# Kernel optimization log

Hardware: AMD Instinct MI355X
Metric: run time of the kernel (lower is better)

Reference implementation:

```python
import jax, jax.numpy as jnp
import numpy as np

K = 3  # hardcoded in TransitionUp.forward

def setup_inputs() -> dict:
    key = jax.random.key(0)
    ks = jax.random.split(key, 8)
    M, N = 32768, 8192
    UP_C, DOWN_C, OUT_C = 128, 256, 128
    return {
        "up_points": jax.random.normal(ks[0], (M, 3), dtype=jnp.float32),
        "up_features": jax.random.normal(ks[1], (M, UP_C), dtype=jnp.float32),
        "down_points": jax.random.normal(ks[2], (N, 3), dtype=jnp.float32),
        "down_features": jax.random.normal(ks[3], (N, DOWN_C), dtype=jnp.float32),
        # torch nn.Linear params: W [out,in], b [out]
        "W_up": jax.random.normal(ks[4], (OUT_C, UP_C), dtype=jnp.float32) / np.sqrt(UP_C),
        "b_up": jax.random.normal(ks[5], (OUT_C,), dtype=jnp.float32) * 0.01,
        "W_down": jax.random.normal(ks[6], (OUT_C, DOWN_C), dtype=jnp.float32) / np.sqrt(DOWN_C),
        "b_down": jax.random.normal(ks[7], (OUT_C,), dtype=jnp.float32) * 0.01,
    }

def interpolate_knn(query_points, dataset_points, dataset_features, k):
    # squared pairwise distances [M, N]
    delta = query_points[:, None, :] - dataset_points[None, :, :]
    dist = jnp.sum(delta * delta, axis=-1)
    neg_dist, knn_idx = jax.lax.top_k(-dist, k)  # smallest-k
    knn_dist = -neg_dist                           # [M, k]
    knn_feats = dataset_features[knn_idx]          # [M, k, C]
    recip = 1.0 / (knn_dist + 1e-8)
    weights = recip / jnp.sum(recip, axis=-1, keepdims=True)  # [M, k]
    return jnp.einsum('mk,mkc->mc', weights, knn_feats)

def reference(up_points, up_features, down_points, down_features, W_up, b_up, W_down, b_down):
    down_f = down_features @ W_down.T + b_down            # [N, OUT_C]
    interp_f = interpolate_knn(up_points, down_points, down_f, K)  # [M, OUT_C]
    return interp_f + (up_features @ W_up.T + b_up)
```

## Files before the change

### kernel.cpp

```cpp
#include <hip/hip_runtime.h>
#include <cfloat>

#define M_UP   32768
#define N_DOWN 8192
#define UPC    128
#define DOWNC  256
#define OUTC   128
#define NCHUNK 8
#define CHUNK  (N_DOWN / NCHUNK)
#define G      8
#define Q      2
#define PG     12

__device__ __forceinline__ void fma4(float4& acc, float s, const float4 w) {
    acc.x = fmaf(s, w.x, acc.x);
    acc.y = fmaf(s, w.y, acc.y);
    acc.z = fmaf(s, w.z, acc.z);
    acc.w = fmaf(s, w.w, acc.w);
}

__device__ __forceinline__ void top3_bl(float s, int idx,
                                        float& d0, float& d1, float& d2,
                                        int& i0, int& i1, int& i2) {
    bool c0 = s < d0, c1 = s < d1, c2 = s < d2;
    float n0 = fminf(d0, s);
    float n1 = __builtin_amdgcn_fmed3f(d0, d1, s);
    float n2 = __builtin_amdgcn_fmed3f(d1, d2, s);
    int m0 = c0 ? idx : i0;
    int m1 = c0 ? i0 : (c1 ? idx : i1);
    int m2 = c1 ? i1 : (c2 ? idx : i2);
    d0 = n0; d1 = n1; d2 = n2;
    i0 = m0; i1 = m1; i2 = m2;
}

__global__ __launch_bounds__(256) void transpose_w(
        const float* __restrict__ W_up, const float* __restrict__ W_down,
        float* __restrict__ wt_up, float* __restrict__ wt_down) {
    int e = blockIdx.x * 256 + threadIdx.x;
    if (e < DOWNC * OUTC) {
        int k = e >> 7, c = e & 127;
        wt_down[e] = W_down[c * DOWNC + k];
    } else {
        int e2 = e - DOWNC * OUTC;
        int k = e2 >> 7, c = e2 & 127;
        wt_up[e2] = W_up[c * UPC + k];
    }
}

__global__ __launch_bounds__(256) void down_proj(
        const float* __restrict__ A, const float* __restrict__ WT,
        const float* __restrict__ bias, float* __restrict__ down_f) {
    __shared__ __align__(16) float sA[16 * DOWNC];
    __shared__ __align__(16) float sW[64 * OUTC];
    {
        const float4* Ab4 = (const float4*)(A + blockIdx.x * 16 * DOWNC);
        float4* sA4 = (float4*)sA;
        #pragma unroll
        for (int i = 0; i < 4; ++i)
            sA4[threadIdx.x + i * 256] = Ab4[threadIdx.x + i * 256];
    }
    const int c4 = threadIdx.x & 31;
    const int rr = threadIdx.x >> 5;
    float4 acc0 = {0.f, 0.f, 0.f, 0.f};
    float4 acc1 = {0.f, 0.f, 0.f, 0.f};
    for (int kh = 0; kh < 4; ++kh) {
        if (kh) __syncthreads();
        {
            const float4* W4 = (const float4*)(WT + kh * 64 * OUTC);
            float4* sW4 = (float4*)sW;
            #pragma unroll
            for (int i = 0; i < 8; ++i)
                sW4[threadIdx.x + i * 256] = W4[threadIdx.x + i * 256];
        }
        __syncthreads();
        #pragma unroll 2
        for (int k2 = 0; k2 < 64; k2 += 4) {
            const int k = kh * 64 + k2;
            float4 a0 = *(const float4*)&sA[rr * DOWNC + k];
            float4 a1 = *(const float4*)&sA[(rr + 8) * DOWNC + k];
            const float4* wp = (const float4*)(sW + k2 * OUTC) + c4;
            float4 w0 = wp[0], w1 = wp[32], w2 = wp[64], w3 = wp[96];
            fma4(acc0, a0.x, w0); fma4(acc0, a0.y, w1);
            fma4(acc0, a0.z, w2); fma4(acc0, a0.w, w3);
            fma4(acc1, a1.x, w0); fma4(acc1, a1.y, w1);
            fma4(acc1, a1.z, w2); fma4(acc1, a1.w, w3);
        }
    }
    const int r0 = blockIdx.x * 16 + rr;
    const int r1 = r0 + 8;
    float4 b = ((const float4*)bias)[c4];
    acc0.x += b.x; acc0.y += b.y; acc0.z += b.z; acc0.w += b.w;
    acc1.x += b.x; acc1.y += b.y; acc1.z += b.z; acc1.w += b.w;
    ((float4*)down_f)[r0 * 32 + c4] = acc0;
    ((float4*)down_f)[r1 * 32 + c4] = acc1;
}

__global__ __launch_bounds__(256) void knn_partial(
        const float* __restrict__ up_points,
        const float* __restrict__ down_points,
        float2* __restrict__ part) {
    __shared__ __align__(16) float sx[PG * (CHUNK / G)];
    __shared__ __align__(16) float sy[PG * (CHUNK / G)];
    __shared__ __align__(16) float sz[PG * (CHUNK / G)];
    const int base = blockIdx.y * CHUNK;
    for (int t = threadIdx.x; t < CHUNK; t += 256) {
        int g = base + t;
        int gi = t >> 3, j = t & 7;
        sx[PG * gi + j] = down_points[3 * g];
        sy[PG * gi + j] = down_points[3 * g + 1];
        sz[PG * gi + j] = down_points[3 * g + 2];
    }
    __syncthreads();

    const int m0 = blockIdx.x * (256 * Q) + threadIdx.x;
    const int m1 = m0 + 256;
    const float q0x = up_points[3 * m0];
    const float q0y = up_points[3 * m0 + 1];
    const float q0z = up_points[3 * m0 + 2];
    const float q1x = up_points[3 * m1];
    const float q1y = up_points[3 * m1 + 1];
    const float q1z = up_points[3 * m1 + 2];

    float a_gd0 = FLT_MAX, a_gd1 = FLT_MAX, a_gd2 = FLT_MAX;
    int   a_gi0 = 0, a_gi1 = 0, a_gi2 = 0;
    float b_gd0 = FLT_MAX, b_gd1 = FLT_MAX, b_gd2 = FLT_MAX;
    int   b_gi0 = 0, b_gi1 = 0, b_gi2 = 0;

    for (int gi = 0; gi < CHUNK / G; ++gi) {
        float4 x0 = *(const float4*)&sx[PG * gi], x1 = *(const float4*)&sx[PG * gi + 4];
        float4 y0 = *(const float4*)&sy[PG * gi], y1 = *(const float4*)&sy[PG * gi + 4];
        float4 z0 = *(const float4*)&sz[PG * gi], z1 = *(const float4*)&sz[PG * gi + 4];
        float px[G] = {x0.x, x0.y, x0.z, x0.w, x1.x, x1.y, x1.z, x1.w};
        float py[G] = {y0.x, y0.y, y0.z, y0.w, y1.x, y1.y, y1.z, y1.w};
        float pz[G] = {z0.x, z0.y, z0.z, z0.w, z1.x, z1.y, z1.z, z1.w};
        float s0[G], s1[G];
        #pragma unroll
        for (int j = 0; j < G; ++j) {
            float dx0 = q0x - px[j], dy0 = q0y - py[j], dz0 = q0z - pz[j];
            s0[j] = fmaf(dz0, dz0, fmaf(dy0, dy0, dx0 * dx0));
            float dx1 = q1x - px[j], dy1 = q1y - py[j], dz1 = q1z - pz[j];
            s1[j] = fmaf(dz1, dz1, fmaf(dy1, dy1, dx1 * dx1));
        }
        float gm0 = fminf(fminf(fminf(s0[0], s0[1]), fminf(s0[2], s0[3])),
                          fminf(fminf(s0[4], s0[5]), fminf(s0[6], s0[7])));
        float gm1 = fminf(fminf(fminf(s1[0], s1[1]), fminf(s1[2], s1[3])),
                          fminf(fminf(s1[4], s1[5]), fminf(s1[6], s1[7])));
        top3_bl(gm0, gi, a_gd0, a_gd1, a_gd2, a_gi0, a_gi1, a_gi2);
        top3_bl(gm1, gi, b_gd0, b_gd1, b_gd2, b_gi0, b_gi1, b_gi2);
    }

    #pragma unroll
    for (int qq = 0; qq < Q; ++qq) {
        const float qx = qq ? q1x : q0x;
        const float qy = qq ? q1y : q0y;
        const float qz = qq ? q1z : q0z;
        int bases[3];
        if (qq == 0) { bases[0] = a_gi0; bases[1] = a_gi1; bases[2] = a_gi2; }
        else         { bases[0] = b_gi0; bases[1] = b_gi1; bases[2] = b_gi2; }
        float D0 = FLT_MAX, D1 = FLT_MAX, D2 = FLT_MAX;
        int I0 = 0, I1 = 0, I2 = 0;
        #pragma unroll
        for (int t = 0; t < 3; ++t) {
            const int gb = bases[t];
            float4 x0 = *(const float4*)&sx[PG * gb], x1 = *(const float4*)&sx[PG * gb + 4];
            float4 y0 = *(const float4*)&sy[PG * gb], y1 = *(const float4*)&sy[PG * gb + 4];
            float4 z0 = *(const float4*)&sz[PG * gb], z1 = *(const float4*)&sz[PG * gb + 4];
            float px[G] = {x0.x, x0.y, x0.z, x0.w, x1.x, x1.y, x1.z, x1.w};
            float py[G] = {y0.x, y0.y, y0.z, y0.w, y1.x, y1.y, y1.z, y1.w};
            float pz[G] = {z0.x, z0.y, z0.z, z0.w, z1.x, z1.y, z1.z, z1.w};
            #pragma unroll
            for (int j = 0; j < G; ++j) {
                float dx = qx - px[j], dy = qy - py[j], dz = qz - pz[j];
                float s = fmaf(dz, dz, fmaf(dy, dy, dx * dx));
                top3_bl(s, base + gb * G + j, D0, D1, D2, I0, I1, I2);
            }
        }
        const int m = qq ? m1 : m0;
        const int o = (blockIdx.y * M_UP + m) * 3;
        part[o]     = make_float2(D0, __int_as_float(I0));
        part[o + 1] = make_float2(D1, __int_as_float(I1));
        part[o + 2] = make_float2(D2, __int_as_float(I2));
    }
}

__global__ __launch_bounds__(256) void up_fused(
        const float* __restrict__ A, const float* __restrict__ WT,
        const float* __restrict__ bias, const float* __restrict__ down_f,
        const float2* __restrict__ part,
        float* __restrict__ out) {
    __shared__ __align__(16) float sA[16 * UPC];
    __shared__ __align__(16) float sW[64 * OUTC];
    {
        const float4* Ab4 = (const float4*)(A + blockIdx.x * 16 * UPC);
        float4* sA4 = (float4*)sA;
        #pragma unroll
        for (int i = 0; i < 2; ++i)
            sA4[threadIdx.x + i * 256] = Ab4[threadIdx.x + i * 256];
    }
    const int c4 = threadIdx.x & 31;
    const int rr = threadIdx.x >> 5;
    const int q0 = blockIdx.x * 16 + rr;
    const int q1 = q0 + 8;
    float4 acc0 = {0.f, 0.f, 0.f, 0.f};
    float4 acc1 = {0.f, 0.f, 0.f, 0.f};
    for (int kh = 0; kh < 2; ++kh) {
        if (kh) __syncthreads();
        {
            const float4* W4 = (const float4*)(WT + kh * 64 * OUTC);
            float4* sW4 = (float4*)sW;
            #pragma unroll
            for (int i = 0; i < 8; ++i)
                sW4[threadIdx.x + i * 256] = W4[threadIdx.x + i * 256];
        }
        __syncthreads();
        #pragma unroll 2
        for (int k2 = 0; k2 < 64; k2 += 4) {
            const int k = kh * 64 + k2;
            float4 a0 = *(const float4*)&sA[rr * UPC + k];
            float4 a1 = *(const float4*)&sA[(rr + 8) * UPC + k];
            const float4* wp = (const float4*)(sW + k2 * OUTC) + c4;
            float4 w0 = wp[0], w1 = wp[32], w2 = wp[64], w3 = wp[96];
            fma4(acc0, a0.x, w0); fma4(acc0, a0.y, w1);
            fma4(acc0, a0.z, w2); fma4(acc0, a0.w, w3);
            fma4(acc1, a1.x, w0); fma4(acc1, a1.y, w1);
            fma4(acc1, a1.z, w2); fma4(acc1, a1.w, w3);
        }
    }
    const float4 b = ((const float4*)bias)[c4];
    const float4* df4 = (const float4*)down_f;
    #pragma unroll
    for (int t = 0; t < 2; ++t) {
        const int q = t ? q1 : q0;
        float4 acc = t ? acc1 : acc0;
        float D0 = FLT_MAX, D1 = FLT_MAX, D2 = FLT_MAX;
        int I0 = 0, I1 = 0, I2 = 0;
        #pragma unroll
        for (int s = 0; s < NCHUNK; ++s) {
            const float2* p = part + (s * M_UP + q) * 3;
            #pragma unroll
            for (int j = 0; j < 3; ++j) {
                float2 v = p[j];
                top3_bl(v.x, __float_as_int(v.y), D0, D1, D2, I0, I1, I2);
            }
        }
        float r0 = 1.f / (D0 + 1e-8f);
        float r1 = 1.f / (D1 + 1e-8f);
        float r2 = 1.f / (D2 + 1e-8f);
        float rs = (r0 + r1) + r2;
        float w0 = r0 / rs, w1 = r1 / rs, w2 = r2 / rs;
        float4 f0 = df4[I0 * 32 + c4];
        float4 f1 = df4[I1 * 32 + c4];
        float4 f2 = df4[I2 * 32 + c4];
        float4 res;
        res.x = acc.x + b.x + fmaf(w0, f0.x, fmaf(w1, f1.x, w2 * f2.x));
        res.y = acc.y + b.y + fmaf(w0, f0.y, fmaf(w1, f1.y, w2 * f2.y));
        res.z = acc.z + b.z + fmaf(w0, f0.z, fmaf(w1, f1.z, w2 * f2.z));
        res.w = acc.w + b.w + fmaf(w0, f0.w, fmaf(w1, f1.w, w2 * f2.w));
        ((float4*)out)[q * 32 + c4] = res;
    }
}

extern "C" void kernel_launch(void* const* d_in, const int* in_sizes, int n_in,
                              void* d_out, int out_size, void* d_ws, size_t ws_size,
                              hipStream_t stream) {
    const float* up_points     = (const float*)d_in[0];
    const float* up_features   = (const float*)d_in[1];
    const float* down_points   = (const float*)d_in[2];
    const float* down_features = (const float*)d_in[3];
    const float* W_up          = (const float*)d_in[4];
    const float* b_up          = (const float*)d_in[5];
    const float* W_down        = (const float*)d_in[6];
    const float* b_down        = (const float*)d_in[7];
    float* out = (float*)d_out;

    float* wt_down = (float*)d_ws;
    float* wt_up   = wt_down + DOWNC * OUTC;
    float* down_f  = wt_up + UPC * OUTC;
    float2* part   = (float2*)(down_f + N_DOWN * OUTC);

    transpose_w<<<(DOWNC * OUTC + UPC * OUTC) / 256, 256, 0, stream>>>(
        W_up, W_down, wt_up, wt_down);
    down_proj<<<N_DOWN / 16, 256, 0, stream>>>(
        down_features, wt_down, b_down, down_f);
    knn_partial<<<dim3(M_UP / (256 * Q), NCHUNK), 256, 0, stream>>>(
        up_points, down_points, part);
    up_fused<<<M_UP / 16, 256, 0, stream>>>(
        up_features, wt_up, b_up, down_f, part, out);
}
```

Baseline: 196.6 us.

## Use 32-row GEMM tiles with 2x8 per-thread register blocking in projections

```diff
diff --git a/kernel.cpp b/kernel.cpp
--- a/kernel.cpp
+++ b/kernel.cpp
@@ -47,52 +47,61 @@
     }
 }
 
+template <int K>
+__device__ __forceinline__ void gemm_tile32(
+        const float* __restrict__ A, const float* __restrict__ WT,
+        float* sA , float* sW ,
+        int rbase, int tid, float4 acc[2][2]) {
+    const int rl = tid & 15;
+    const int c0 = (tid >> 4) * 8;
+    #pragma unroll 1
+    for (int ph = 0; ph < K / 32; ++ph) {
+        if (ph) __syncthreads();
+        {
+            int r = tid >> 3, k4 = tid & 7;
+            float4 v = *(const float4*)(A + (size_t)(rbase + r) * K + ph * 32 + k4 * 4);
+            *(float4*)&sA[r * 36 + k4 * 4] = v;
+        }
+        #pragma unroll
+        for (int i = 0; i < 4; ++i) {
+            int idx = tid + i * 256;
+            int kk = idx >> 5, cc = idx & 31;
+            float4 v = *(const float4*)(WT + (size_t)(ph * 32 + kk) * OUTC + cc * 4);
+            *(float4*)&sW[kk * OUTC + cc * 4] = v;
+        }
+        __syncthreads();
+        #pragma unroll 4
+        for (int kk = 0; kk < 32; ++kk) {
+            float a0 = sA[rl * 36 + kk];
+            float a1 = sA[(rl + 16) * 36 + kk];
+            float4 w0 = *(const float4*)&sW[kk * OUTC + c0];
+            float4 w1 = *(const float4*)&sW[kk * OUTC + c0 + 4];
+            fma4(acc[0][0], a0, w0); fma4(acc[0][1], a0, w1);
+            fma4(acc[1][0], a1, w0); fma4(acc[1][1], a1, w1);
+        }
+    }
+}
+
 __global__ __launch_bounds__(256) void down_proj(
         const float* __restrict__ A, const float* __restrict__ WT,
         const float* __restrict__ bias, float* __restrict__ down_f) {
-    __shared__ __align__(16) float sA[16 * DOWNC];
-    __shared__ __align__(16) float sW[64 * OUTC];
-    {
-        const float4* Ab4 = (const float4*)(A + blockIdx.x * 16 * DOWNC);
-        float4* sA4 = (float4*)sA;
-        #pragma unroll
-        for (int i = 0; i < 4; ++i)
-            sA4[threadIdx.x + i * 256] = Ab4[threadIdx.x + i * 256];
-    }
-    const int c4 = threadIdx.x & 31;
-    const int rr = threadIdx.x >> 5;
-    float4 acc0 = {0.f, 0.f, 0.f, 0.f};
-    float4 acc1 = {0.f, 0.f, 0.f, 0.f};
-    for (int kh = 0; kh < 4; ++kh) {
-        if (kh) __syncthreads();
-        {
-            const float4* W4 = (const float4*)(WT + kh * 64 * OUTC);
-            float4* sW4 = (float4*)sW;
-            #pragma unroll
-            for (int i = 0; i < 8; ++i)
-                sW4[threadIdx.x + i * 256] = W4[threadIdx.x + i * 256];
-        }
-        __syncthreads();
-        #pragma unroll 2
-        for (int k2 = 0; k2 < 64; k2 += 4) {
-            const int k = kh * 64 + k2;
-            float4 a0 = *(const float4*)&sA[rr * DOWNC + k];
-            float4 a1 = *(const float4*)&sA[(rr + 8) * DOWNC + k];
-            const float4* wp = (const float4*)(sW + k2 * OUTC) + c4;
-            float4 w0 = wp[0], w1 = wp[32], w2 = wp[64], w3 = wp[96];
-            fma4(acc0, a0.x, w0); fma4(acc0, a0.y, w1);
-            fma4(acc0, a0.z, w2); fma4(acc0, a0.w, w3);
-            fma4(acc1, a1.x, w0); fma4(acc1, a1.y, w1);
-            fma4(acc1, a1.z, w2); fma4(acc1, a1.w, w3);
-        }
-    }
-    const int r0 = blockIdx.x * 16 + rr;
-    const int r1 = r0 + 8;
-    float4 b = ((const float4*)bias)[c4];
-    acc0.x += b.x; acc0.y += b.y; acc0.z += b.z; acc0.w += b.w;
-    acc1.x += b.x; acc1.y += b.y; acc1.z += b.z; acc1.w += b.w;
-    ((float4*)down_f)[r0 * 32 + c4] = acc0;
-    ((float4*)down_f)[r1 * 32 + c4] = acc1;
+    __shared__ __align__(16) float sA[32 * 36];
+    __shared__ __align__(16) float sW[32 * OUTC];
+    float4 acc[2][2] = {};
+    gemm_tile32<DOWNC>(A, WT, sA, sW, blockIdx.x * 32, threadIdx.x, acc);
+    const int rl = threadIdx.x & 15;
+    const int cg = (threadIdx.x >> 4) * 2;
+    const float4 b0 = ((const float4*)bias)[cg];
+    const float4 b1 = ((const float4*)bias)[cg + 1];
+    #pragma unroll
+    for (int i = 0; i < 2; ++i) {
+        const int row = blockIdx.x * 32 + rl + 16 * i;
+        float4 v0 = acc[i][0], v1 = acc[i][1];
+        v0.x += b0.x; v0.y += b0.y; v0.z += b0.z; v0.w += b0.w;
+        v1.x += b1.x; v1.y += b1.y; v1.z += b1.z; v1.w += b1.w;
+        ((float4*)down_f)[row * 32 + cg] = v0;
+        ((float4*)down_f)[row * 32 + cg + 1] = v1;
+    }
 }
 
 __global__ __launch_bounds__(256) void knn_partial(
@@ -188,55 +197,24 @@
         const float* __restrict__ bias, const float* __restrict__ down_f,
         const float2* __restrict__ part,
         float* __restrict__ out) {
-    __shared__ __align__(16) float sA[16 * UPC];
-    __shared__ __align__(16) float sW[64 * OUTC];
-    {
-        const float4* Ab4 = (const float4*)(A + blockIdx.x * 16 * UPC);
-        float4* sA4 = (float4*)sA;
-        #pragma unroll
-        for (int i = 0; i < 2; ++i)
-            sA4[threadIdx.x + i * 256] = Ab4[threadIdx.x + i * 256];
-    }
-    const int c4 = threadIdx.x & 31;
-    const int rr = threadIdx.x >> 5;
-    const int q0 = blockIdx.x * 16 + rr;
-    const int q1 = q0 + 8;
-    float4 acc0 = {0.f, 0.f, 0.f, 0.f};
-    float4 acc1 = {0.f, 0.f, 0.f, 0.f};
-    for (int kh = 0; kh < 2; ++kh) {
-        if (kh) __syncthreads();
-        {
-            const float4* W4 = (const float4*)(WT + kh * 64 * OUTC);
-            float4* sW4 = (float4*)sW;
-            #pragma unroll
-            for (int i = 0; i < 8; ++i)
-                sW4[threadIdx.x + i * 256] = W4[threadIdx.x + i * 256];
-        }
-        __syncthreads();
-        #pragma unroll 2
-        for (int k2 = 0; k2 < 64; k2 += 4) {
-            const int k = kh * 64 + k2;
-            float4 a0 = *(const float4*)&sA[rr * UPC + k];
-            float4 a1 = *(const float4*)&sA[(rr + 8) * UPC + k];
-            const float4* wp = (const float4*)(sW + k2 * OUTC) + c4;
-            float4 w0 = wp[0], w1 = wp[32], w2 = wp[64], w3 = wp[96];
-            fma4(acc0, a0.x, w0); fma4(acc0, a0.y, w1);
-            fma4(acc0, a0.z, w2); fma4(acc0, a0.w, w3);
-            fma4(acc1, a1.x, w0); fma4(acc1, a1.y, w1);
-            fma4(acc1, a1.z, w2); fma4(acc1, a1.w, w3);
-        }
-    }
-    const float4 b = ((const float4*)bias)[c4];
+    __shared__ __align__(16) float sA[32 * 36];
+    __shared__ __align__(16) float sW[32 * OUTC];
+    float4 acc[2][2] = {};
+    gemm_tile32<UPC>(A, WT, sA, sW, blockIdx.x * 32, threadIdx.x, acc);
+
+    const int rl = threadIdx.x & 15;
+    const int cg = (threadIdx.x >> 4) * 2;
+    const float4 b0 = ((const float4*)bias)[cg];
+    const float4 b1 = ((const float4*)bias)[cg + 1];
     const float4* df4 = (const float4*)down_f;
     #pragma unroll
-    for (int t = 0; t < 2; ++t) {
-        const int q = t ? q1 : q0;
-        float4 acc = t ? acc1 : acc0;
+    for (int i = 0; i < 2; ++i) {
+        const int m = blockIdx.x * 32 + rl + 16 * i;
         float D0 = FLT_MAX, D1 = FLT_MAX, D2 = FLT_MAX;
         int I0 = 0, I1 = 0, I2 = 0;
         #pragma unroll
         for (int s = 0; s < NCHUNK; ++s) {
-            const float2* p = part + (s * M_UP + q) * 3;
+            const float2* p = part + (s * M_UP + m) * 3;
             #pragma unroll
             for (int j = 0; j < 3; ++j) {
                 float2 v = p[j];
@@ -248,15 +226,21 @@
         float r2 = 1.f / (D2 + 1e-8f);
         float rs = (r0 + r1) + r2;
         float w0 = r0 / rs, w1 = r1 / rs, w2 = r2 / rs;
-        float4 f0 = df4[I0 * 32 + c4];
-        float4 f1 = df4[I1 * 32 + c4];
-        float4 f2 = df4[I2 * 32 + c4];
-        float4 res;
-        res.x = acc.x + b.x + fmaf(w0, f0.x, fmaf(w1, f1.x, w2 * f2.x));
-        res.y = acc.y + b.y + fmaf(w0, f0.y, fmaf(w1, f1.y, w2 * f2.y));
-        res.z = acc.z + b.z + fmaf(w0, f0.z, fmaf(w1, f1.z, w2 * f2.z));
-        res.w = acc.w + b.w + fmaf(w0, f0.w, fmaf(w1, f1.w, w2 * f2.w));
-        ((float4*)out)[q * 32 + c4] = res;
+        float4 f00 = df4[I0 * 32 + cg],     f01 = df4[I0 * 32 + cg + 1];
+        float4 f10 = df4[I1 * 32 + cg],     f11 = df4[I1 * 32 + cg + 1];
+        float4 f20 = df4[I2 * 32 + cg],     f21 = df4[I2 * 32 + cg + 1];
+        float4 v0 = acc[i][0], v1 = acc[i][1];
+        float4 res0, res1;
+        res0.x = v0.x + b0.x + fmaf(w0, f00.x, fmaf(w1, f10.x, w2 * f20.x));
+        res0.y = v0.y + b0.y + fmaf(w0, f00.y, fmaf(w1, f10.y, w2 * f20.y));
+        res0.z = v0.z + b0.z + fmaf(w0, f00.z, fmaf(w1, f10.z, w2 * f20.z));
+        res0.w = v0.w + b0.w + fmaf(w0, f00.w, fmaf(w1, f10.w, w2 * f20.w));
+        res1.x = v1.x + b1.x + fmaf(w0, f01.x, fmaf(w1, f11.x, w2 * f21.x));
+        res1.y = v1.y + b1.y + fmaf(w0, f01.y, fmaf(w1, f11.y, w2 * f21.y));
+        res1.z = v1.z + b1.z + fmaf(w0, f01.z, fmaf(w1, f11.z, w2 * f21.z));
+        res1.w = v1.w + b1.w + fmaf(w0, f01.w, fmaf(w1, f11.w, w2 * f21.w));
+        ((float4*)out)[m * 32 + cg] = res0;
+        ((float4*)out)[m * 32 + cg + 1] = res1;
     }
 }
 
@@ -280,10 +264,10 @@
 
     transpose_w<<<(DOWNC * OUTC + UPC * OUTC) / 256, 256, 0, stream>>>(
         W_up, W_down, wt_up, wt_down);
-    down_proj<<<N_DOWN / 16, 256, 0, stream>>>(
+    down_proj<<<N_DOWN / 32, 256, 0, stream>>>(
         down_features, wt_down, b_down, down_f);
     knn_partial<<<dim3(M_UP / (256 * Q), NCHUNK), 256, 0, stream>>>(
         up_points, down_points, part);
-    up_fused<<<M_UP / 16, 256, 0, stream>>>(
+    up_fused<<<M_UP / 32, 256, 0, stream>>>(
         up_features, wt_up, b_up, down_f, part, out);
 }
```

Measured after the change: 188.2 us. -4.3%, faster.
